# Performance work log

Measured on AMD Instinct MI355X. Metric: run time of the kernel, lower is better.

The kernel has to match this reference:

```python
import jax, jax.numpy as jnp
import numpy as np

B, IN, OUT = 4096, 1024, 1024


def setup_inputs() -> dict:
    key = jax.random.key(0)
    ks = jax.random.split(key, 11)
    xav = 1.0 / np.sqrt(IN + OUT)  # Xavier-style scale for sigmoid/tanh layers
    d = {
        "x": jax.random.normal(ks[0], (B, IN), dtype=jnp.float32),
        "h": jax.random.normal(ks[1], (B, OUT), dtype=jnp.float32),
        "c": jax.random.normal(ks[2], (B, OUT), dtype=jnp.float32),
        "w_f": jax.random.normal(ks[3], (IN + OUT, OUT), dtype=jnp.float32) * xav,
        "b_f": jnp.zeros((1, OUT), dtype=jnp.float32),
        "w_i": jax.random.normal(ks[4], (IN + OUT, OUT), dtype=jnp.float32) * xav,
        "b_i": jnp.zeros((1, OUT), dtype=jnp.float32),
        "w_c": jax.random.normal(ks[5], (IN + OUT, OUT), dtype=jnp.float32) * xav,
        "b_c": jnp.zeros((1, OUT), dtype=jnp.float32),
        "w_o": jax.random.normal(ks[6], (IN + OUT, OUT), dtype=jnp.float32) * xav,
        "b_o": jnp.zeros((1, OUT), dtype=jnp.float32),
    }
    return d


def reference(x, h, c, w_f, b_f, w_i, b_i, w_c, b_c, w_o, b_o):
    # combined input [B, IN+OUT]
    z = jnp.concatenate([x, h], axis=1)
    f = jax.nn.sigmoid(z @ w_f + b_f)      # forget gate
    i = jax.nn.sigmoid(z @ w_i + b_i)      # update (input) gate
    g = jnp.tanh(z @ w_c + b_c)            # candidate cell
    o = jax.nn.sigmoid(z @ w_o + b_o)      # output gate
    c_new = c * f + i * g
    h_new = jnp.tanh(c_new) * o
    return h_new
```

## Files before the change

### kernel.cpp

```cpp
#include <hip/hip_runtime.h>
#include <hip/hip_bf16.h>

typedef short short8 __attribute__((ext_vector_type(8)));
typedef float f32x4 __attribute__((ext_vector_type(4)));

#define NB 4096
#define KZ 2048
#define NG 1024
#define NKS 32

__device__ __forceinline__ unsigned short f2bf(float f) {
  unsigned int u = __float_as_uint(f);
  u += 0x7FFFu + ((u >> 16) & 1u);
  return (unsigned short)(u >> 16);
}
__device__ __forceinline__ float bf2f(unsigned short s) {
  return __uint_as_float(((unsigned int)s) << 16);
}
__device__ __forceinline__ void gload_lds16(const void* g, void* l) {
  __builtin_amdgcn_global_load_lds(
      (__attribute__((address_space(1))) void*)g,
      (__attribute__((address_space(3))) void*)l, 16, 0, 0);
}
__device__ __forceinline__ float sigm(float x) { return 1.f / (1.f + __expf(-x)); }
__device__ __forceinline__ float tanh_fast(float x) {
  float e = __expf(-2.f * fabsf(x));
  float r = (1.f - e) / (1.f + e);
  return copysignf(r, x);
}

__global__ void zsplit_kernel(const float* __restrict__ x, const float* __restrict__ h,
                              unsigned short* __restrict__ zh) {
  int idx = blockIdx.x * 256 + threadIdx.x;
  int e = idx << 2;
  int r = e >> 11;
  int k = e & (KZ - 1);
  const float* src = (k < 1024) ? (x + ((size_t)r << 10) + k)
                                : (h + ((size_t)r << 10) + (k - 1024));
  float4 v = *reinterpret_cast<const float4*>(src);
  float vf[4] = {v.x, v.y, v.z, v.w};
  unsigned short hh[4];
#pragma unroll
  for (int j = 0; j < 4; ++j) hh[j] = f2bf(vf[j]);
  uint2 H = make_uint2((unsigned)hh[0] | ((unsigned)hh[1] << 16),
                       (unsigned)hh[2] | ((unsigned)hh[3] << 16));
  *reinterpret_cast<uint2*>(zh + e) = H;
}

__global__ void wsplit_kernel(const float* __restrict__ w0, const float* __restrict__ w1,
                              const float* __restrict__ w2, const float* __restrict__ w3,
                              unsigned short* __restrict__ wh, unsigned short* __restrict__ wl) {
  __shared__ float tile[32][33];
  int g = blockIdx.z;
  const float* w = (g == 0) ? w0 : (g == 1) ? w1 : (g == 2) ? w2 : w3;
  int k0 = blockIdx.x << 5;
  int n0 = blockIdx.y << 5;
  int t = threadIdx.x;
  int rk = t >> 3, q = t & 7;
  float4 v = *reinterpret_cast<const float4*>(w + (size_t)(k0 + rk) * NG + n0 + (q << 2));
  tile[rk][(q << 2) + 0] = v.x;
  tile[rk][(q << 2) + 1] = v.y;
  tile[rk][(q << 2) + 2] = v.z;
  tile[rk][(q << 2) + 3] = v.w;
  __syncthreads();
  int n = t >> 3, kq = t & 7;
  unsigned short hs[4], ls[4];
#pragma unroll
  for (int j = 0; j < 4; ++j) {
    float f = tile[(kq << 2) + j][n];
    unsigned short hi = f2bf(f);
    unsigned short lo = f2bf(f - bf2f(hi));
    hs[j] = hi; ls[j] = lo;
  }
  int nn = n0 + n;
  int p = ((nn >> 6) << 8) | (((nn >> 4) & 3) << 6) | (g << 4) | (nn & 15);
  size_t o = (size_t)p * KZ + k0 + (kq << 2);
  uint2 H = make_uint2((unsigned)hs[0] | ((unsigned)hs[1] << 16),
                       (unsigned)hs[2] | ((unsigned)hs[3] << 16));
  uint2 L = make_uint2((unsigned)ls[0] | ((unsigned)ls[1] << 16),
                       (unsigned)ls[2] | ((unsigned)ls[3] << 16));
  *reinterpret_cast<uint2*>(wh + o) = H;
  *reinterpret_cast<uint2*>(wl + o) = L;
}

#define MFMA(a, b, c) __builtin_amdgcn_mfma_f32_16x16x32_bf16((a), (b), (c), 0, 0, 0)
#define BAR() __builtin_amdgcn_s_barrier()
#define LGKM0() asm volatile("s_waitcnt lgkmcnt(0)" ::: "memory")
#define PRIO1() __builtin_amdgcn_s_setprio(1)
#define PRIO0() __builtin_amdgcn_s_setprio(0)

__global__ __launch_bounds__(512, 2) void lstm_gemm256_kernel(
    const unsigned short* __restrict__ zh,
    const unsigned short* __restrict__ wh, const unsigned short* __restrict__ wl,
    const float* __restrict__ c_in, const float* __restrict__ bf_,
    const float* __restrict__ bi_, const float* __restrict__ bc_,
    const float* __restrict__ bo_, float* __restrict__ out) {
  __shared__ unsigned short As[2 * 16384];
  __shared__ unsigned short Bh[16384];
  __shared__ unsigned short Bl[16384];
  const int t = threadIdx.x;
  const int lane = t & 63;
  const int wid = t >> 6;
  const int wr = wid >> 2;
  const int wc = wid & 3;
  const int l15 = lane & 15;
  const int l4 = lane >> 4;

  const int bid = blockIdx.x;
  const int swz = ((bid & 7) << 5) + (bid >> 3);
  const int bx = swz & 15;
  const int by = swz >> 4;
  const int brow0 = by << 8;
  const int pcol0 = bx << 8;

  char* AsB = (char*)As;
  char* BhB = (char*)Bh;
  char* BlB = (char*)Bl;

  int aoff[2], boff[2];
#pragma unroll
  for (int j = 0; j < 2; ++j) {
    int row = (j << 6) + (t >> 3);
    int sl = (t & 7) ^ (row & 7);
    aoff[j] = (brow0 + row) * KZ + (sl << 3);
    boff[j] = (pcol0 + row) * KZ + (sl << 3);
  }
  const int ldsw = wid << 10;

  auto STAGE = [&](int ks, int hx) {
    if (ks >= NKS) return;
    const int kk = ks << 6;
    if (hx < 2) {
      const int lb = ((ks & 1) << 15) + (hx << 14);
#pragma unroll
      for (int j = 0; j < 2; ++j)
        gload_lds16(zh + aoff[j] + hx * (128 * KZ) + kk, AsB + lb + (j << 13) + ldsw);
    } else if (hx < 4) {
      const int h = hx - 2;
#pragma unroll
      for (int j = 0; j < 2; ++j)
        gload_lds16(wh + boff[j] + h * (128 * KZ) + kk, BhB + (h << 14) + (j << 13) + ldsw);
    } else {
      const int h = hx - 4;
#pragma unroll
      for (int j = 0; j < 2; ++j)
        gload_lds16(wl + boff[j] + h * (128 * KZ) + kk, BlB + (h << 14) + (j << 13) + ldsw);
    }
  };

  f32x4 acc[8][4];
#pragma unroll
  for (int m = 0; m < 8; ++m)
#pragma unroll
    for (int n = 0; n < 4; ++n) acc[m][n] = (f32x4){0.f, 0.f, 0.f, 0.f};

  const int rx = l15 & 7;
  const int sx0 = (l4 ^ rx) << 4;
  const int sx1 = ((4 + l4) ^ rx) << 4;
  const int aB = l15 << 7;
  const int bB = ((wc & 1) << 13) + (l15 << 7);
  const int aW = wr << 14;
  const int bW = (wc >> 1) << 14;

  short8 a0[8], a1[8], bh0[4], bh1[4], bl0[4], bl1[4];

  STAGE(0, 0); STAGE(0, 1); STAGE(0, 2); STAGE(0, 3); STAGE(0, 4); STAGE(0, 5);
  asm volatile("s_waitcnt vmcnt(4)" ::: "memory");
  BAR();

  for (int ks = 0; ks < NKS; ++ks) {
    const int abase = ((ks & 1) << 15) + aW;
    const bool last = (ks == NKS - 1);

#pragma unroll
    for (int m = 0; m < 4; ++m)
      a0[m] = *reinterpret_cast<const short8*>(AsB + abase + aB + (m << 11) + sx0);
#pragma unroll
    for (int n = 0; n < 4; ++n)
      bh0[n] = *reinterpret_cast<const short8*>(BhB + bW + bB + (n << 11) + sx0);
    BAR(); LGKM0(); PRIO1();
#pragma unroll
    for (int m = 0; m < 4; ++m)
#pragma unroll
      for (int n = 0; n < 4; ++n) acc[m][n] = MFMA(a0[m], bh0[n], acc[m][n]);
    PRIO0(); BAR();

#pragma unroll
    for (int m = 4; m < 8; ++m)
      a0[m] = *reinterpret_cast<const short8*>(AsB + abase + aB + (m << 11) + sx0);
    BAR(); LGKM0(); PRIO1();
#pragma unroll
    for (int m = 0; m < 4; ++m)
#pragma unroll
      for (int n = 0; n < 4; ++n) acc[m + 4][n] = MFMA(a0[m + 4], bh0[n], acc[m + 4][n]);
    PRIO0(); BAR();

#pragma unroll
    for (int m = 0; m < 4; ++m)
      a1[m] = *reinterpret_cast<const short8*>(AsB + abase + aB + (m << 11) + sx1);
#pragma unroll
    for (int n = 0; n < 4; ++n)
      bh1[n] = *reinterpret_cast<const short8*>(BhB + bW + bB + (n << 11) + sx1);
    STAGE(ks + 1, 0);
    BAR(); LGKM0(); PRIO1();
#pragma unroll
    for (int m = 0; m < 4; ++m)
#pragma unroll
      for (int n = 0; n < 4; ++n) acc[m][n] = MFMA(a1[m], bh1[n], acc[m][n]);
    PRIO0(); BAR();

#pragma unroll
    for (int m = 4; m < 8; ++m)
      a1[m] = *reinterpret_cast<const short8*>(AsB + abase + aB + (m << 11) + sx1);
    STAGE(ks + 1, 1);
    if (!last) { asm volatile("s_waitcnt vmcnt(4)" ::: "memory"); }
    else       { asm volatile("s_waitcnt vmcnt(0)" ::: "memory"); }
    BAR(); LGKM0(); PRIO1();
#pragma unroll
    for (int m = 0; m < 4; ++m)
#pragma unroll
      for (int n = 0; n < 4; ++n) acc[m + 4][n] = MFMA(a1[m + 4], bh1[n], acc[m + 4][n]);
    PRIO0(); BAR();

#pragma unroll
    for (int n = 0; n < 4; ++n)
      bl0[n] = *reinterpret_cast<const short8*>(BlB + bW + bB + (n << 11) + sx0);
    STAGE(ks + 1, 2);
    BAR(); LGKM0(); PRIO1();
#pragma unroll
    for (int m = 0; m < 4; ++m)
#pragma unroll
      for (int n = 0; n < 4; ++n) acc[m][n] = MFMA(a0[m], bl0[n], acc[m][n]);
    PRIO0(); BAR();

#pragma unroll
    for (int n = 0; n < 4; ++n)
      bl1[n] = *reinterpret_cast<const short8*>(BlB + bW + bB + (n << 11) + sx1);
    STAGE(ks + 1, 3);
    BAR(); LGKM0(); PRIO1();
#pragma unroll
    for (int m = 0; m < 4; ++m)
#pragma unroll
      for (int n = 0; n < 4; ++n) acc[m + 4][n] = MFMA(a0[m + 4], bl0[n], acc[m + 4][n]);
    PRIO0(); BAR();

    STAGE(ks + 1, 4);
    BAR(); PRIO1();
#pragma unroll
    for (int m = 0; m < 4; ++m)
#pragma unroll
      for (int n = 0; n < 4; ++n) acc[m][n] = MFMA(a1[m], bl1[n], acc[m][n]);
    PRIO0(); BAR();

    STAGE(ks + 1, 5);
    if (!last) { asm volatile("s_waitcnt vmcnt(4)" ::: "memory"); }
    BAR(); PRIO1();
#pragma unroll
    for (int m = 0; m < 4; ++m)
#pragma unroll
      for (int n = 0; n < 4; ++n) acc[m + 4][n] = MFMA(a1[m + 4], bl1[n], acc[m + 4][n]);
    PRIO0(); BAR();
  }

  const int ng = (bx << 6) + (wc << 4) + l15;
  const float vbf = bf_[ng], vbi = bi_[ng], vbc = bc_[ng], vbo = bo_[ng];
#pragma unroll
  for (int m = 0; m < 8; ++m) {
#pragma unroll
    for (int r = 0; r < 4; ++r) {
      const int row = brow0 + (wr << 7) + (m << 4) + (l4 << 2) + r;
      const float fp = acc[m][0][r] + vbf;
      const float ip = acc[m][1][r] + vbi;
      const float gp = acc[m][2][r] + vbc;
      const float op = acc[m][3][r] + vbo;
      const float co = c_in[(size_t)row * NG + ng];
      const float cnew = co * sigm(fp) + sigm(ip) * tanh_fast(gp);
      out[(size_t)row * NG + ng] = tanh_fast(cnew) * sigm(op);
    }
  }
}

extern "C" void kernel_launch(void* const* d_in, const int* in_sizes, int n_in,
                              void* d_out, int out_size, void* d_ws, size_t ws_size,
                              hipStream_t stream) {
  const float* x   = (const float*)d_in[0];
  const float* h   = (const float*)d_in[1];
  const float* c   = (const float*)d_in[2];
  const float* w_f = (const float*)d_in[3];
  const float* b_f = (const float*)d_in[4];
  const float* w_i = (const float*)d_in[5];
  const float* b_i = (const float*)d_in[6];
  const float* w_c = (const float*)d_in[7];
  const float* b_c = (const float*)d_in[8];
  const float* w_o = (const float*)d_in[9];
  const float* b_o = (const float*)d_in[10];
  float* out = (float*)d_out;

  unsigned short* zh = (unsigned short*)d_ws;
  unsigned short* wh = zh + (size_t)NB * KZ;
  unsigned short* wl = wh + (size_t)KZ * 4096;

  zsplit_kernel<<<(NB * KZ / 4) / 256, 256, 0, stream>>>(x, h, zh);
  wsplit_kernel<<<dim3(KZ / 32, NG / 32, 4), 256, 0, stream>>>(w_f, w_i, w_c, w_o, wh, wl);
  lstm_gemm256_kernel<<<256, 512, 0, stream>>>(zh, wh, wl, c,
                                               b_f, b_i, b_c, b_o, out);
}
```

Baseline: 130.5 us.

## Reschedule LSTM GEMM main loop with fewer barriers and partial LDS waits

```diff
diff --git a/kernel.cpp b/kernel.cpp
--- a/kernel.cpp
+++ b/kernel.cpp
@@ -84,8 +84,10 @@
 }
 
 #define MFMA(a, b, c) __builtin_amdgcn_mfma_f32_16x16x32_bf16((a), (b), (c), 0, 0, 0)
-#define BAR() __builtin_amdgcn_s_barrier()
-#define LGKM0() asm volatile("s_waitcnt lgkmcnt(0)" ::: "memory")
+#define ABAR() asm volatile("s_barrier" ::: "memory")
+#define LGKM(N) asm volatile("s_waitcnt lgkmcnt(" #N ")" ::: "memory")
+#define VMC0() asm volatile("s_waitcnt vmcnt(0)" ::: "memory")
+#define SB() __builtin_amdgcn_sched_barrier(0)
 #define PRIO1() __builtin_amdgcn_s_setprio(1)
 #define PRIO0() __builtin_amdgcn_s_setprio(0)
 
@@ -127,24 +129,24 @@
   }
   const int ldsw = wid << 10;
 
-  auto STAGE = [&](int ks, int hx) {
-    if (ks >= NKS) return;
-    const int kk = ks << 6;
+  auto STAGE = [&](int s, int hx) {
+    if (s >= NKS) return;
+    const int kk = s << 6;
     if (hx < 2) {
-      const int lb = ((ks & 1) << 15) + (hx << 14);
+      const int lb = ((s & 1) << 15) + (hx << 14);
 #pragma unroll
       for (int j = 0; j < 2; ++j)
         gload_lds16(zh + aoff[j] + hx * (128 * KZ) + kk, AsB + lb + (j << 13) + ldsw);
     } else if (hx < 4) {
-      const int h = hx - 2;
+      const int hq = hx - 2;
 #pragma unroll
       for (int j = 0; j < 2; ++j)
-        gload_lds16(wh + boff[j] + h * (128 * KZ) + kk, BhB + (h << 14) + (j << 13) + ldsw);
+        gload_lds16(wh + boff[j] + hq * (128 * KZ) + kk, BhB + (hq << 14) + (j << 13) + ldsw);
     } else {
-      const int h = hx - 4;
+      const int hq = hx - 4;
 #pragma unroll
       for (int j = 0; j < 2; ++j)
-        gload_lds16(wl + boff[j] + h * (128 * KZ) + kk, BlB + (h << 14) + (j << 13) + ldsw);
+        gload_lds16(wl + boff[j] + hq * (128 * KZ) + kk, BlB + (hq << 14) + (j << 13) + ldsw);
     }
   };
 
@@ -162,104 +164,109 @@
   const int aW = wr << 14;
   const int bW = (wc >> 1) << 14;
 
-  short8 a0[8], a1[8], bh0[4], bh1[4], bl0[4], bl1[4];
+  short8 aL0[4], aH0[4], aL1[4], aH1[4], vbh0[4], vbh1[4], vbl0[4], vbl1[4];
 
   STAGE(0, 0); STAGE(0, 1); STAGE(0, 2); STAGE(0, 3); STAGE(0, 4); STAGE(0, 5);
-  asm volatile("s_waitcnt vmcnt(4)" ::: "memory");
-  BAR();
+  VMC0();
+  ABAR();
 
   for (int ks = 0; ks < NKS; ++ks) {
     const int abase = ((ks & 1) << 15) + aW;
-    const bool last = (ks == NKS - 1);
-
-#pragma unroll
-    for (int m = 0; m < 4; ++m)
-      a0[m] = *reinterpret_cast<const short8*>(AsB + abase + aB + (m << 11) + sx0);
+
+#pragma unroll
+    for (int m = 0; m < 4; ++m)
+      aL0[m] = *reinterpret_cast<const short8*>(AsB + abase + aB + (m << 11) + sx0);
 #pragma unroll
     for (int n = 0; n < 4; ++n)
-      bh0[n] = *reinterpret_cast<const short8*>(BhB + bW + bB + (n << 11) + sx0);
-    BAR(); LGKM0(); PRIO1();
-#pragma unroll
-    for (int m = 0; m < 4; ++m)
-#pragma unroll
-      for (int n = 0; n < 4; ++n) acc[m][n] = MFMA(a0[m], bh0[n], acc[m][n]);
-    PRIO0(); BAR();
-
-#pragma unroll
-    for (int m = 4; m < 8; ++m)
-      a0[m] = *reinterpret_cast<const short8*>(AsB + abase + aB + (m << 11) + sx0);
-    BAR(); LGKM0(); PRIO1();
-#pragma unroll
-    for (int m = 0; m < 4; ++m)
-#pragma unroll
-      for (int n = 0; n < 4; ++n) acc[m + 4][n] = MFMA(a0[m + 4], bh0[n], acc[m + 4][n]);
-    PRIO0(); BAR();
-
-#pragma unroll
-    for (int m = 0; m < 4; ++m)
-      a1[m] = *reinterpret_cast<const short8*>(AsB + abase + aB + (m << 11) + sx1);
+      vbh0[n] = *reinterpret_cast<const short8*>(BhB + bW + bB + (n << 11) + sx0);
+    SB();
 #pragma unroll
     for (int n = 0; n < 4; ++n)
-      bh1[n] = *reinterpret_cast<const short8*>(BhB + bW + bB + (n << 11) + sx1);
+      vbl0[n] = *reinterpret_cast<const short8*>(BlB + bW + bB + (n << 11) + sx0);
+    SB();
     STAGE(ks + 1, 0);
-    BAR(); LGKM0(); PRIO1();
-#pragma unroll
-    for (int m = 0; m < 4; ++m)
-#pragma unroll
-      for (int n = 0; n < 4; ++n) acc[m][n] = MFMA(a1[m], bh1[n], acc[m][n]);
-    PRIO0(); BAR();
-
-#pragma unroll
-    for (int m = 4; m < 8; ++m)
-      a1[m] = *reinterpret_cast<const short8*>(AsB + abase + aB + (m << 11) + sx1);
+    LGKM(4); SB();
+    PRIO1();
+#pragma unroll
+    for (int m = 0; m < 4; ++m)
+#pragma unroll
+      for (int n = 0; n < 4; ++n) acc[m][n] = MFMA(aL0[m], vbh0[n], acc[m][n]);
+    PRIO0();
+
+#pragma unroll
+    for (int m = 0; m < 4; ++m)
+      aH0[m] = *reinterpret_cast<const short8*>(AsB + abase + aB + ((m + 4) << 11) + sx0);
+    SB();
     STAGE(ks + 1, 1);
-    if (!last) { asm volatile("s_waitcnt vmcnt(4)" ::: "memory"); }
-    else       { asm volatile("s_waitcnt vmcnt(0)" ::: "memory"); }
-    BAR(); LGKM0(); PRIO1();
-#pragma unroll
-    for (int m = 0; m < 4; ++m)
-#pragma unroll
-      for (int n = 0; n < 4; ++n) acc[m + 4][n] = MFMA(a1[m + 4], bh1[n], acc[m + 4][n]);
-    PRIO0(); BAR();
-
+    LGKM(4); SB();
+    PRIO1();
+#pragma unroll
+    for (int m = 0; m < 4; ++m)
+#pragma unroll
+      for (int n = 0; n < 4; ++n) acc[m][n] = MFMA(aL0[m], vbl0[n], acc[m][n]);
+    PRIO0();
+
+#pragma unroll
+    for (int m = 0; m < 4; ++m)
+      aL1[m] = *reinterpret_cast<const short8*>(AsB + abase + aB + (m << 11) + sx1);
 #pragma unroll
     for (int n = 0; n < 4; ++n)
-      bl0[n] = *reinterpret_cast<const short8*>(BlB + bW + bB + (n << 11) + sx0);
-    STAGE(ks + 1, 2);
-    BAR(); LGKM0(); PRIO1();
-#pragma unroll
-    for (int m = 0; m < 4; ++m)
-#pragma unroll
-      for (int n = 0; n < 4; ++n) acc[m][n] = MFMA(a0[m], bl0[n], acc[m][n]);
-    PRIO0(); BAR();
+      vbh1[n] = *reinterpret_cast<const short8*>(BhB + bW + bB + (n << 11) + sx1);
+    SB();
+    LGKM(8); SB();
+    PRIO1();
+#pragma unroll
+    for (int m = 0; m < 4; ++m)
+#pragma unroll
+      for (int n = 0; n < 4; ++n) acc[m + 4][n] = MFMA(aH0[m], vbh0[n], acc[m + 4][n]);
+    PRIO0();
 
 #pragma unroll
     for (int n = 0; n < 4; ++n)
-      bl1[n] = *reinterpret_cast<const short8*>(BlB + bW + bB + (n << 11) + sx1);
-    STAGE(ks + 1, 3);
-    BAR(); LGKM0(); PRIO1();
-#pragma unroll
-    for (int m = 0; m < 4; ++m)
-#pragma unroll
-      for (int n = 0; n < 4; ++n) acc[m + 4][n] = MFMA(a0[m + 4], bl0[n], acc[m + 4][n]);
-    PRIO0(); BAR();
-
-    STAGE(ks + 1, 4);
-    BAR(); PRIO1();
-#pragma unroll
-    for (int m = 0; m < 4; ++m)
-#pragma unroll
-      for (int n = 0; n < 4; ++n) acc[m][n] = MFMA(a1[m], bl1[n], acc[m][n]);
-    PRIO0(); BAR();
-
-    STAGE(ks + 1, 5);
-    if (!last) { asm volatile("s_waitcnt vmcnt(4)" ::: "memory"); }
-    BAR(); PRIO1();
-#pragma unroll
-    for (int m = 0; m < 4; ++m)
-#pragma unroll
-      for (int n = 0; n < 4; ++n) acc[m + 4][n] = MFMA(a1[m + 4], bl1[n], acc[m + 4][n]);
-    PRIO0(); BAR();
+      vbl1[n] = *reinterpret_cast<const short8*>(BlB + bW + bB + (n << 11) + sx1);
+    SB();
+    PRIO1();
+#pragma unroll
+    for (int m = 0; m < 4; ++m)
+#pragma unroll
+      for (int n = 0; n < 4; ++n) acc[m + 4][n] = MFMA(aH0[m], vbl0[n], acc[m + 4][n]);
+    PRIO0();
+
+    LGKM(0); SB();
+    ABAR();
+    STAGE(ks + 1, 2); STAGE(ks + 1, 3); STAGE(ks + 1, 4); STAGE(ks + 1, 5);
+    PRIO1();
+#pragma unroll
+    for (int m = 0; m < 4; ++m)
+#pragma unroll
+      for (int n = 0; n < 4; ++n) acc[m][n] = MFMA(aL1[m], vbh1[n], acc[m][n]);
+    PRIO0();
+
+#pragma unroll
+    for (int m = 0; m < 4; ++m)
+      aH1[m] = *reinterpret_cast<const short8*>(AsB + abase + aB + ((m + 4) << 11) + sx1);
+    SB();
+    PRIO1();
+#pragma unroll
+    for (int m = 0; m < 4; ++m)
+#pragma unroll
+      for (int n = 0; n < 4; ++n) acc[m][n] = MFMA(aL1[m], vbl1[n], acc[m][n]);
+    PRIO0();
+
+    LGKM(0); SB();
+    PRIO1();
+#pragma unroll
+    for (int m = 0; m < 4; ++m)
+#pragma unroll
+      for (int n = 0; n < 4; ++n) acc[m + 4][n] = MFMA(aH1[m], vbh1[n], acc[m + 4][n]);
+#pragma unroll
+    for (int m = 0; m < 4; ++m)
+#pragma unroll
+      for (int n = 0; n < 4; ++n) acc[m + 4][n] = MFMA(aH1[m], vbl1[n], acc[m + 4][n]);
+    PRIO0();
+
+    VMC0(); SB();
+    ABAR();
   }
 
   const int ng = (bx << 6) + (wc << 4) + l15;
```

Result: no change. 131.4 us (+0.7%).

## Reschedule Bl-tile loads into current iteration and split A fragments into halves

Applied to the files above, without the earlier changes.

```diff
diff --git a/kernel.cpp b/kernel.cpp
--- a/kernel.cpp
+++ b/kernel.cpp
@@ -127,24 +127,24 @@
   }
   const int ldsw = wid << 10;
 
-  auto STAGE = [&](int ks, int hx) {
-    if (ks >= NKS) return;
-    const int kk = ks << 6;
+  auto STAGE = [&](int s, int hx) {
+    if (s >= NKS) return;
+    const int kk = s << 6;
     if (hx < 2) {
-      const int lb = ((ks & 1) << 15) + (hx << 14);
+      const int lb = ((s & 1) << 15) + (hx << 14);
 #pragma unroll
       for (int j = 0; j < 2; ++j)
         gload_lds16(zh + aoff[j] + hx * (128 * KZ) + kk, AsB + lb + (j << 13) + ldsw);
     } else if (hx < 4) {
-      const int h = hx - 2;
+      const int hq = hx - 2;
 #pragma unroll
       for (int j = 0; j < 2; ++j)
-        gload_lds16(wh + boff[j] + h * (128 * KZ) + kk, BhB + (h << 14) + (j << 13) + ldsw);
+        gload_lds16(wh + boff[j] + hq * (128 * KZ) + kk, BhB + (hq << 14) + (j << 13) + ldsw);
     } else {
-      const int h = hx - 4;
+      const int hq = hx - 4;
 #pragma unroll
       for (int j = 0; j < 2; ++j)
-        gload_lds16(wl + boff[j] + h * (128 * KZ) + kk, BlB + (h << 14) + (j << 13) + ldsw);
+        gload_lds16(wl + boff[j] + hq * (128 * KZ) + kk, BlB + (hq << 14) + (j << 13) + ldsw);
     }
   };
 
@@ -162,10 +162,10 @@
   const int aW = wr << 14;
   const int bW = (wc >> 1) << 14;
 
-  short8 a0[8], a1[8], bh0[4], bh1[4], bl0[4], bl1[4];
-
-  STAGE(0, 0); STAGE(0, 1); STAGE(0, 2); STAGE(0, 3); STAGE(0, 4); STAGE(0, 5);
-  asm volatile("s_waitcnt vmcnt(4)" ::: "memory");
+  short8 aL0[4], aH0[4], aL1[4], aH1[4], bh0[4], bh1[4], bl0[4], bl1[4];
+
+  STAGE(0, 0); STAGE(0, 1); STAGE(0, 2); STAGE(0, 3);
+  asm volatile("s_waitcnt vmcnt(0)" ::: "memory");
   BAR();
 
   for (int ks = 0; ks < NKS; ++ks) {
@@ -174,30 +174,32 @@
 
 #pragma unroll
     for (int m = 0; m < 4; ++m)
-      a0[m] = *reinterpret_cast<const short8*>(AsB + abase + aB + (m << 11) + sx0);
+      aL0[m] = *reinterpret_cast<const short8*>(AsB + abase + aB + (m << 11) + sx0);
 #pragma unroll
     for (int n = 0; n < 4; ++n)
       bh0[n] = *reinterpret_cast<const short8*>(BhB + bW + bB + (n << 11) + sx0);
-    BAR(); LGKM0(); PRIO1();
-#pragma unroll
-    for (int m = 0; m < 4; ++m)
-#pragma unroll
-      for (int n = 0; n < 4; ++n) acc[m][n] = MFMA(a0[m], bh0[n], acc[m][n]);
-    PRIO0(); BAR();
-
-#pragma unroll
-    for (int m = 4; m < 8; ++m)
-      a0[m] = *reinterpret_cast<const short8*>(AsB + abase + aB + (m << 11) + sx0);
-    BAR(); LGKM0(); PRIO1();
-#pragma unroll
-    for (int m = 0; m < 4; ++m)
-#pragma unroll
-      for (int n = 0; n < 4; ++n) acc[m + 4][n] = MFMA(a0[m + 4], bh0[n], acc[m + 4][n]);
-    PRIO0(); BAR();
-
-#pragma unroll
-    for (int m = 0; m < 4; ++m)
-      a1[m] = *reinterpret_cast<const short8*>(AsB + abase + aB + (m << 11) + sx1);
+    STAGE(ks, 4);
+    BAR(); LGKM0(); PRIO1();
+#pragma unroll
+    for (int m = 0; m < 4; ++m)
+#pragma unroll
+      for (int n = 0; n < 4; ++n) acc[m][n] = MFMA(aL0[m], bh0[n], acc[m][n]);
+    PRIO0(); BAR();
+
+#pragma unroll
+    for (int m = 0; m < 4; ++m)
+      aH0[m] = *reinterpret_cast<const short8*>(AsB + abase + aB + ((m + 4) << 11) + sx0);
+    STAGE(ks, 5);
+    BAR(); LGKM0(); PRIO1();
+#pragma unroll
+    for (int m = 0; m < 4; ++m)
+#pragma unroll
+      for (int n = 0; n < 4; ++n) acc[m + 4][n] = MFMA(aH0[m], bh0[n], acc[m + 4][n]);
+    PRIO0(); BAR();
+
+#pragma unroll
+    for (int m = 0; m < 4; ++m)
+      aL1[m] = *reinterpret_cast<const short8*>(AsB + abase + aB + (m << 11) + sx1);
 #pragma unroll
     for (int n = 0; n < 4; ++n)
       bh1[n] = *reinterpret_cast<const short8*>(BhB + bW + bB + (n << 11) + sx1);
@@ -206,12 +208,12 @@
 #pragma unroll
     for (int m = 0; m < 4; ++m)
 #pragma unroll
-      for (int n = 0; n < 4; ++n) acc[m][n] = MFMA(a1[m], bh1[n], acc[m][n]);
-    PRIO0(); BAR();
-
-#pragma unroll
-    for (int m = 4; m < 8; ++m)
-      a1[m] = *reinterpret_cast<const short8*>(AsB + abase + aB + (m << 11) + sx1);
+      for (int n = 0; n < 4; ++n) acc[m][n] = MFMA(aL1[m], bh1[n], acc[m][n]);
+    PRIO0(); BAR();
+
+#pragma unroll
+    for (int m = 0; m < 4; ++m)
+      aH1[m] = *reinterpret_cast<const short8*>(AsB + abase + aB + ((m + 4) << 11) + sx1);
     STAGE(ks + 1, 1);
     if (!last) { asm volatile("s_waitcnt vmcnt(4)" ::: "memory"); }
     else       { asm volatile("s_waitcnt vmcnt(0)" ::: "memory"); }
@@ -219,7 +221,7 @@
 #pragma unroll
     for (int m = 0; m < 4; ++m)
 #pragma unroll
-      for (int n = 0; n < 4; ++n) acc[m + 4][n] = MFMA(a1[m + 4], bh1[n], acc[m + 4][n]);
+      for (int n = 0; n < 4; ++n) acc[m + 4][n] = MFMA(aH1[m], bh1[n], acc[m + 4][n]);
     PRIO0(); BAR();
 
 #pragma unroll
@@ -230,35 +232,33 @@
 #pragma unroll
     for (int m = 0; m < 4; ++m)
 #pragma unroll
-      for (int n = 0; n < 4; ++n) acc[m][n] = MFMA(a0[m], bl0[n], acc[m][n]);
+      for (int n = 0; n < 4; ++n) acc[m][n] = MFMA(aL0[m], bl0[n], acc[m][n]);
+    PRIO0(); BAR();
+
+    STAGE(ks + 1, 3);
+    BAR(); PRIO1();
+#pragma unroll
+    for (int m = 0; m < 4; ++m)
+#pragma unroll
+      for (int n = 0; n < 4; ++n) acc[m + 4][n] = MFMA(aH0[m], bl0[n], acc[m + 4][n]);
     PRIO0(); BAR();
 
 #pragma unroll
     for (int n = 0; n < 4; ++n)
       bl1[n] = *reinterpret_cast<const short8*>(BlB + bW + bB + (n << 11) + sx1);
-    STAGE(ks + 1, 3);
-    BAR(); LGKM0(); PRIO1();
-#pragma unroll
-    for (int m = 0; m < 4; ++m)
-#pragma unroll
-      for (int n = 0; n < 4; ++n) acc[m + 4][n] = MFMA(a0[m + 4], bl0[n], acc[m + 4][n]);
-    PRIO0(); BAR();
-
-    STAGE(ks + 1, 4);
+    BAR(); LGKM0(); PRIO1();
+#pragma unroll
+    for (int m = 0; m < 4; ++m)
+#pragma unroll
+      for (int n = 0; n < 4; ++n) acc[m][n] = MFMA(aL1[m], bl1[n], acc[m][n]);
+    PRIO0(); BAR();
+
+    asm volatile("s_waitcnt vmcnt(0)" ::: "memory");
     BAR(); PRIO1();
 #pragma unroll
     for (int m = 0; m < 4; ++m)
 #pragma unroll
-      for (int n = 0; n < 4; ++n) acc[m][n] = MFMA(a1[m], bl1[n], acc[m][n]);
-    PRIO0(); BAR();
-
-    STAGE(ks + 1, 5);
-    if (!last) { asm volatile("s_waitcnt vmcnt(4)" ::: "memory"); }
-    BAR(); PRIO1();
-#pragma unroll
-    for (int m = 0; m < 4; ++m)
-#pragma unroll
-      for (int n = 0; n < 4; ++n) acc[m + 4][n] = MFMA(a1[m + 4], bl1[n], acc[m + 4][n]);
+      for (int n = 0; n < 4; ++n) acc[m + 4][n] = MFMA(aH1[m], bl1[n], acc[m + 4][n]);
     PRIO0(); BAR();
   }
 
```

Result: slower. 137.0 us (+5.0%).
